# Performance work log

Hardware: AMD Instinct MI355X
Metric: run time of the kernel (lower is better)

## Reference

```python
import jax, jax.numpy as jnp
from jax import lax
import numpy as np

THRESHOLD = 1.25
CURRENT_DECAY = 0.25
VOLTAGE_DECAY = 0.03
TAU_GRAD = 0.03
SCALE_GRAD = 3.0


@jax.custom_vjp
def spike_fn(v):
    # Heaviside spike on membrane voltage (threshold already subtracted)
    return (v >= 0.0).astype(v.dtype)

def _spike_fwd(v):
    return spike_fn(v), v

def _spike_bwd(v, g):
    # slayer-style exponential surrogate gradient around threshold
    surrogate = SCALE_GRAD * jnp.exp(-jnp.abs(v) / TAU_GRAD)
    return (g * surrogate,)

spike_fn.defvjp(_spike_fwd, _spike_bwd)


def cuba_dense(x, v_w, g_w, delay):
    """x: [B, C_in, T] spikes -> [B, C_out, T] spikes.
    Weight-normalized dense synapse + CUBA leaky-integrate-and-fire scan + axonal delay."""
    # weight norm: W = g * v / ||v||_row
    norm = jnp.sqrt(jnp.sum(v_w * v_w, axis=1, keepdims=True))
    W = g_w[:, None] * v_w / norm                       # [O, C]
    z = jnp.einsum('bct,oc->bot', x, W)                 # synaptic current input [B, O, T]
    B, O, T = z.shape
    zT = jnp.transpose(z, (2, 0, 1))                    # [T, B, O]

    def step(carry, zt):
        cur, vol = carry
        cur = cur * (1.0 - CURRENT_DECAY) + zt
        vol = vol * (1.0 - VOLTAGE_DECAY) + cur
        s = spike_fn(vol - THRESHOLD)
        vol = vol * (1.0 - s)                           # reset to zero on spike
        return (cur, vol), s

    init = (jnp.zeros((B, O), z.dtype), jnp.zeros((B, O), z.dtype))
    _, sT = lax.scan(step, init, zT)                    # [T, B, O]
    s = jnp.transpose(sT, (1, 2, 0))                    # [B, O, T]

    # per-neuron integer axonal delay: out[b,n,t] = s[b,n,t-d_n]
    t_idx = jnp.arange(T)[None, :] - delay[:, None]     # [O, T]
    valid = (t_idx >= 0)
    gathered = s[:, jnp.arange(O)[:, None], jnp.clip(t_idx, 0, T - 1)]
    return jnp.where(valid[None, :, :], gathered, jnp.zeros((), s.dtype))


def setup_inputs() -> dict:
    key = jax.random.key(0)
    ks = jax.random.split(key, 10)
    B, C, T = 32, 34 * 34 * 2, 300
    spike = (jax.random.uniform(ks[0], (B, C, T)) < 0.1).astype(jnp.float32)
    v1 = jax.random.normal(ks[1], (512, C), jnp.float32) * 0.1
    g1 = jax.random.uniform(ks[2], (512,), jnp.float32) + 0.5
    v2 = jax.random.normal(ks[3], (512, 512), jnp.float32) * 0.1
    g2 = jax.random.uniform(ks[4], (512,), jnp.float32) + 0.5
    v3 = jax.random.normal(ks[5], (10, 512), jnp.float32) * 0.1
    g3 = jax.random.uniform(ks[6], (10,), jnp.float32) + 0.5
    d1 = jax.random.randint(ks[7], (512,), 0, 8, jnp.int32)
    d2 = jax.random.randint(ks[8], (512,), 0, 8, jnp.int32)
    d3 = jax.random.randint(ks[9], (10,), 0, 8, jnp.int32)
    return {"spike": spike, "v1": v1, "g1": g1, "v2": v2, "g2": g2,
            "v3": v3, "g3": g3, "d1": d1, "d2": d2, "d3": d3}


def reference(spike, v1, g1, v2, g2, v3, g3, d1, d2, d3):
    s1 = cuba_dense(spike, v1, g1, d1)
    s2 = cuba_dense(s1, v2, g2, d2)
    s3 = cuba_dense(s2, v3, g3, d3)
    counts = jnp.stack([jnp.mean(s1), jnp.mean(s2), jnp.mean(s3)]).reshape(1, -1)
    return s3, counts
```

## Files before the change

kernel.cpp:

```cpp
#include <hip/hip_runtime.h>

#define B_   32
#define T_   300
#define C1_  2312
#define O1_  512
#define O2_  512
#define O3_  10
#define M_   (B_*T_)
#define KSPLIT_ 1152


__global__ void calc_f(const float* __restrict__ v, const float* __restrict__ g,
                       double* __restrict__ f, int O, int C) {
    int o = blockIdx.x;
    const float* row = v + (size_t)o * C;
    double s = 0.0;
    for (int c = threadIdx.x; c < C; c += blockDim.x) {
        double x = (double)row[c];
        s += x * x;
    }
    for (int off = 32; off; off >>= 1) s += __shfl_down(s, off);
    __shared__ double wsum[4];
    int lane = threadIdx.x & 63, wv = threadIdx.x >> 6;
    if (lane == 0) wsum[wv] = s;
    __syncthreads();
    if (threadIdx.x == 0) {
        double tot = 0.0;
        for (int i = 0; i < (int)(blockDim.x >> 6); ++i) tot += wsum[i];
        f[o] = (double)g[o] / sqrt(tot);
    }
}

__global__ void transpose_scale(const float* __restrict__ v, const double* __restrict__ f,
                                double* __restrict__ wt, int O, int C, int ldo) {
    __shared__ double tile[32][33];
    int c0 = blockIdx.x * 32, o0 = blockIdx.y * 32;
    int tx = threadIdx.x, ty = threadIdx.y;
    for (int k = 0; k < 4; ++k) {
        int o = o0 + ty + k * 8, c = c0 + tx;
        double val = 0.0;
        if (o < O && c < C) val = (double)v[(size_t)o * C + c] * f[o];
        tile[ty + k * 8][tx] = val;
    }
    __syncthreads();
    for (int k = 0; k < 4; ++k) {
        int c = c0 + ty + k * 8, o = o0 + tx;
        if (c < C && o < O) wt[(size_t)c * ldo + o] = tile[tx][ty + k * 8];
    }
}

__global__ void build_bits(const float* __restrict__ X, unsigned* __restrict__ bits) {
    size_t idx = (size_t)blockIdx.x * 256 + threadIdx.x;
    if (idx >= (size_t)B_ * C1_ * 10) return;
    int t32 = (int)(idx % 10);
    size_t bc = idx / 10;
    const float* src = X + bc * T_ + t32 * 32;
    int nq = (t32 == 9) ? 3 : 8;
    unsigned m = 0;
    for (int q = 0; q < nq; ++q) {
        float4 v = *(const float4*)(src + q * 4);
        if (v.x != 0.f) m |= 1u << (q * 4 + 0);
        if (v.y != 0.f) m |= 1u << (q * 4 + 1);
        if (v.z != 0.f) m |= 1u << (q * 4 + 2);
        if (v.w != 0.f) m |= 1u << (q * 4 + 3);
    }
    bits[idx] = m;
}

__global__ __launch_bounds__(512, 4) void gemm1(const unsigned* __restrict__ Xbits,
                                                const double* __restrict__ Wt,
                                                double* __restrict__ Z0,
                                                double* __restrict__ Z1) {
    __shared__ double Ws[2][16][256];
    int n = blockIdx.x;
    int combo = n & 3;
    int khalf = combo & 1;
    int o0 = (combo >> 1) * 256;
    int i = n >> 2;
    int tb = i % 10;
    int bpair = i / 10;
    int tid = threadIdx.x;
    int w = tid >> 6;
    int lane = tid & 63;
    int b = bpair * 2 + (w >> 2);
    int w8s = __builtin_amdgcn_readfirstlane((w & 3) << 3);
    int cbeg = khalf ? KSPLIT_ : 0;
    int qend = khalf ? C1_ : KSPLIT_;
    const int NT = khalf ? 73 : 72;
    double* __restrict__ Z = khalf ? Z1 : Z0;
    double acc[8][4];
#pragma unroll
    for (int tj = 0; tj < 8; ++tj)
#pragma unroll
        for (int i2 = 0; i2 < 4; ++i2) acc[tj][i2] = 0.0;
    const unsigned* xbp = Xbits + (size_t)b * C1_ * 10 + tb;

    double2 wreg[4];
    unsigned mval, mvaln = 0u;

    auto load_w = [&](int c0) {
#pragma unroll
        for (int h = 0; h < 4; ++h) {
            int idx = h * 512 + tid;
            int r = idx >> 7, od = (idx & 127) * 2;
            int c = c0 + r;
            double2 val; val.x = 0.0; val.y = 0.0;
            if (c < qend) val = *(const double2*)(Wt + (size_t)c * O1_ + o0 + od);
            wreg[h] = val;
        }
    };
    auto load_m = [&](int c0) -> unsigned {
        int c = c0 + lane;
        return (lane < 16 && c < qend) ? xbp[(size_t)c * 10] : 0u;
    };
    auto store_w = [&](int bi) {
#pragma unroll
        for (int h = 0; h < 4; ++h) {
            int idx = h * 512 + tid;
            int r = idx >> 7, od = (idx & 127) * 2;
            *(double2*)(&Ws[bi][r][od]) = wreg[h];
        }
    };

    load_w(cbeg);
    mval = load_m(cbeg);
    store_w(0);
    __syncthreads();
    int cur = 0;
    for (int tile = 0; tile < NT; ++tile) {
        if (tile + 1 < NT) {
            int cn = cbeg + (tile + 1) * 16;
            load_w(cn);
            mvaln = load_m(cn);
        }
#pragma unroll
        for (int k = 0; k < 16; ++k) {
            unsigned smk = (unsigned)__builtin_amdgcn_readlane((int)mval, k);
            unsigned soct = (smk >> w8s) & 0xffu;
            if (soct) {
                double wf[4];
#pragma unroll
                for (int i2 = 0; i2 < 4; ++i2) wf[i2] = Ws[cur][k][lane + 64 * i2];
#pragma unroll
                for (int tj = 0; tj < 8; ++tj) {
                    if (soct & (1u << tj)) {
#pragma unroll
                        for (int i2 = 0; i2 < 4; ++i2) acc[tj][i2] += wf[i2];
                    }
                }
            }
        }
        if (tile + 1 < NT) {
            store_w(cur ^ 1);
            __syncthreads();
        }
        mval = mvaln;
        cur ^= 1;
    }
#pragma unroll
    for (int tj = 0; tj < 8; ++tj) {
        int t = tb * 32 + w8s + tj;
        if (t < T_) {
            double* dst = Z + ((size_t)b * T_ + t) * O1_ + o0;
#pragma unroll
            for (int i2 = 0; i2 < 4; ++i2)
                dst[lane + 64 * i2] = acc[tj][i2];
        }
    }
}

__global__ __launch_bounds__(512, 4) void gemm2s(const unsigned* __restrict__ Sbits,
                                                 const double* __restrict__ Wt,
                                                 double* __restrict__ Z0,
                                                 double* __restrict__ Z1) {
    __shared__ double Ws[2][16][256];
    int n = blockIdx.x;
    int combo = n & 3;
    int khalf = combo & 1;
    int o0 = (combo >> 1) * 256;
    int i = n >> 2;
    int twin = i % 5;
    int b = i / 5;
    int tid = threadIdx.x;
    int w = tid >> 6;
    int lane = tid & 63;
    int w8s = __builtin_amdgcn_readfirstlane((w & 3) << 3);
    int word = twin * 2 + (w >> 2);
    int cbeg = khalf * 256;
    double* __restrict__ Z = khalf ? Z1 : Z0;
    double acc[8][4];
#pragma unroll
    for (int tj = 0; tj < 8; ++tj)
#pragma unroll
        for (int i2 = 0; i2 < 4; ++i2) acc[tj][i2] = 0.0;
    const unsigned* xbp = Sbits + (size_t)b * O1_ * 10 + word;

    double2 wreg[4];
    unsigned mval, mvaln = 0u;

    auto load_w = [&](int c0) {
#pragma unroll
        for (int h = 0; h < 4; ++h) {
            int idx = h * 512 + tid;
            int r = idx >> 7, od = (idx & 127) * 2;
            int c = c0 + r;
            wreg[h] = *(const double2*)(Wt + (size_t)c * O2_ + o0 + od);
        }
    };
    auto load_m = [&](int c0) -> unsigned {
        int c = c0 + lane;
        return (lane < 16) ? xbp[(size_t)c * 10] : 0u;
    };
    auto store_w = [&](int bi) {
#pragma unroll
        for (int h = 0; h < 4; ++h) {
            int idx = h * 512 + tid;
            int r = idx >> 7, od = (idx & 127) * 2;
            *(double2*)(&Ws[bi][r][od]) = wreg[h];
        }
    };

    load_w(cbeg);
    mval = load_m(cbeg);
    store_w(0);
    __syncthreads();
    int cur = 0;
    for (int tile = 0; tile < 16; ++tile) {
        if (tile + 1 < 16) {
            int cn = cbeg + (tile + 1) * 16;
            load_w(cn);
            mvaln = load_m(cn);
        }
#pragma unroll
        for (int k = 0; k < 16; ++k) {
            unsigned smk = (unsigned)__builtin_amdgcn_readlane((int)mval, k);
            unsigned soct = (smk >> w8s) & 0xffu;
            if (soct) {
                double wf[4];
#pragma unroll
                for (int i2 = 0; i2 < 4; ++i2) wf[i2] = Ws[cur][k][lane + 64 * i2];
#pragma unroll
                for (int tj = 0; tj < 8; ++tj) {
                    if (soct & (1u << tj)) {
#pragma unroll
                        for (int i2 = 0; i2 < 4; ++i2) acc[tj][i2] += wf[i2];
                    }
                }
            }
        }
        if (tile + 1 < 16) {
            store_w(cur ^ 1);
            __syncthreads();
        }
        mval = mvaln;
        cur ^= 1;
    }
#pragma unroll
    for (int tj = 0; tj < 8; ++tj) {
        int t = twin * 64 + w * 8 + tj;
        if (t < T_) {
            double* dst = Z + ((size_t)b * T_ + t) * O2_ + o0;
#pragma unroll
            for (int i2 = 0; i2 < 4; ++i2)
                dst[lane + 64 * i2] = acc[tj][i2];
        }
    }
}

__global__ void gemm3(const float* __restrict__ A,
                      const double* __restrict__ Wt,
                      double* __restrict__ Z) {
    __shared__ double w[512 * 16];
    for (int e = threadIdx.x; e < 4096; e += 256)
        ((double2*)w)[e] = ((const double2*)Wt)[e];
    __syncthreads();
    int m = blockIdx.x * 256 + threadIdx.x;
    if (m >= M_) return;
    double acc[O3_];
#pragma unroll
    for (int o = 0; o < O3_; ++o) acc[o] = 0.0;
    const float4* Ar = (const float4*)(A + (size_t)m * 512);
    for (int cq = 0; cq < 128; ++cq) {
        float4 a = Ar[cq];
        float av[4] = {a.x, a.y, a.z, a.w};
#pragma unroll
        for (int u = 0; u < 4; ++u)
#pragma unroll
            for (int o = 0; o < O3_; ++o) acc[o] += (double)av[u] * w[(cq * 4 + u) * 16 + o];
    }
    double* dst = Z + (size_t)m * 16;
#pragma unroll
    for (int o = 0; o < O3_; ++o) dst[o] = acc[o];
}

__global__ void scan12(const double* __restrict__ Za,
                       const double* __restrict__ Zb,
                       const int* __restrict__ delay,
                       float* __restrict__ Sout,
                       unsigned* __restrict__ bitsOut,
                       float* __restrict__ sumOut) {
    int blk = blockIdx.x;
    int o = (blk & 7) * 64 + threadIdx.x;
    int b = blk >> 3;
    size_t base = (size_t)b * T_ * O1_ + o;
    const double* z  = Za + base;
    const double* z2 = Zb ? Zb + base : nullptr;
    float* s = Sout ? Sout + base : nullptr;
    int d = delay[o];
    if (s) for (int t = 0; t < d; ++t) s[(size_t)t * O1_] = 0.f;
    double cur = 0.0, vol = 0.0;
    float cnt = 0.f;
    unsigned bw = 0u;
    for (int t8 = 0; t8 < 296; t8 += 8) {
        double zbuf[8];
#pragma unroll
        for (int u = 0; u < 8; ++u) zbuf[u] = z[(size_t)(t8 + u) * O1_];
        if (z2) {
#pragma unroll
            for (int u = 0; u < 8; ++u) zbuf[u] += z2[(size_t)(t8 + u) * O1_];
        }
#pragma unroll
        for (int u = 0; u < 8; ++u) {
            int t = t8 + u;
            cur = cur * 0.75 + zbuf[u];
            vol = vol * 0.97 + cur;
            float sp = (vol >= 1.25) ? 1.f : 0.f;
            if (sp > 0.f) vol = 0.0;
            int tw = t + d;
            if (tw < T_) {
                if (s) s[(size_t)tw * O1_] = sp;
                cnt += sp;
                if (bitsOut) {
                    if (sp > 0.f) bw |= 1u << (tw & 31);
                    if ((tw & 31) == 31) { bitsOut[((size_t)b * O1_ + o) * 10 + (tw >> 5)] = bw; bw = 0u; }
                }
            }
        }
    }
    {
        double zbuf[4];
#pragma unroll
        for (int u = 0; u < 4; ++u) zbuf[u] = z[(size_t)(296 + u) * O1_];
        if (z2) {
#pragma unroll
            for (int u = 0; u < 4; ++u) zbuf[u] += z2[(size_t)(296 + u) * O1_];
        }
#pragma unroll
        for (int u = 0; u < 4; ++u) {
            int t = 296 + u;
            cur = cur * 0.75 + zbuf[u];
            vol = vol * 0.97 + cur;
            float sp = (vol >= 1.25) ? 1.f : 0.f;
            if (sp > 0.f) vol = 0.0;
            int tw = t + d;
            if (tw < T_) {
                if (s) s[(size_t)tw * O1_] = sp;
                cnt += sp;
                if (bitsOut) {
                    if (sp > 0.f) bw |= 1u << (tw & 31);
                    if ((tw & 31) == 31) { bitsOut[((size_t)b * O1_ + o) * 10 + (tw >> 5)] = bw; bw = 0u; }
                }
            }
        }
    }
    if (bitsOut) bitsOut[((size_t)b * O1_ + o) * 10 + 9] = bw;
    for (int off = 32; off; off >>= 1) cnt += __shfl_down(cnt, off);
    if (threadIdx.x == 0) atomicAdd(sumOut, cnt);
}

__global__ void scan3(const double* __restrict__ Z3,
                      const int* __restrict__ d3,
                      float* __restrict__ out,
                      float* __restrict__ sumOut) {
    __shared__ double zt[T_ * 16];
    int b = blockIdx.x;
    const double2* src = (const double2*)(Z3 + (size_t)b * T_ * 16);
    for (int e = threadIdx.x; e < T_ * 8; e += 64)
        ((double2*)zt)[e] = src[e];
    __syncthreads();
    int o = threadIdx.x;
    if (o < O3_) {
        int d = d3[o];
        float* dst = out + (size_t)b * O3_ * T_ + (size_t)o * T_;
        for (int t = 0; t < d; ++t) dst[t] = 0.f;
        double cur = 0.0, vol = 0.0;
        float cnt = 0.f;
        for (int t = 0; t < T_; ++t) {
            cur = cur * 0.75 + zt[t * 16 + o];
            vol = vol * 0.97 + cur;
            float sp = (vol >= 1.25) ? 1.f : 0.f;
            if (sp > 0.f) vol = 0.0;
            int tw = t + d;
            if (tw < T_) { dst[tw] = sp; cnt += sp; }
        }
        atomicAdd(sumOut, cnt);
    }
}

__global__ void finalize(const float* __restrict__ sums, float* __restrict__ out) {
    if (threadIdx.x == 0) {
        out[0] = (float)((double)sums[0] / (double)(B_ * O1_ * T_));
        out[1] = (float)((double)sums[1] / (double)(B_ * O2_ * T_));
        out[2] = (float)((double)sums[2] / (double)(B_ * O3_ * T_));
    }
}

extern "C" void kernel_launch(void* const* d_in, const int* in_sizes, int n_in,
                              void* d_out, int out_size, void* d_ws, size_t ws_size,
                              hipStream_t stream) {
    const float* spike = (const float*)d_in[0];
    const float* v1 = (const float*)d_in[1];
    const float* g1 = (const float*)d_in[2];
    const float* v2 = (const float*)d_in[3];
    const float* g2 = (const float*)d_in[4];
    const float* v3 = (const float*)d_in[5];
    const float* g3 = (const float*)d_in[6];
    const int* d1 = (const int*)d_in[7];
    const int* d2 = (const int*)d_in[8];
    const int* d3 = (const int*)d_in[9];
    float* out = (float*)d_out;

    double* dw = (double*)d_ws;
    size_t off = 0;
    double* f1  = dw + off; off += 512;
    double* f2  = dw + off; off += 512;
    double* f3  = dw + off; off += 16;
    double* Wt1 = dw + off; off += (size_t)C1_ * O1_;
    double* Wt2 = dw + off; off += 512 * 512;
    double* Wt3 = dw + off; off += 512 * 16;
    double* zA  = dw + off; off += (size_t)M_ * 512;
    double* zB  = dw + off; off += (size_t)M_ * 512;
    double* z3b = dw + off; off += (size_t)M_ * 16;
    float* fw = (float*)(dw + off);
    float* sB    = fw;
    float* sums  = fw + (size_t)M_ * 512;
    unsigned* Xbits = (unsigned*)(fw + (size_t)M_ * 512 + 4);
    unsigned* bits2 = Xbits + (size_t)B_ * C1_ * 10;
    (void)ws_size; (void)out_size; (void)in_sizes; (void)n_in;

    hipMemsetAsync(sums, 0, 4 * sizeof(float), stream);

    build_bits<<<(B_ * C1_ * 10 + 255) / 256, 256, 0, stream>>>(spike, Xbits);

    calc_f<<<512, 256, 0, stream>>>(v1, g1, f1, O1_, C1_);
    calc_f<<<512, 256, 0, stream>>>(v2, g2, f2, O2_, O1_);
    calc_f<<<O3_, 256, 0, stream>>>(v3, g3, f3, O3_, O2_);

    transpose_scale<<<dim3((C1_ + 31) / 32, 16), dim3(32, 8), 0, stream>>>(v1, f1, Wt1, O1_, C1_, O1_);
    transpose_scale<<<dim3(16, 16), dim3(32, 8), 0, stream>>>(v2, f2, Wt2, O2_, O1_, O2_);
    transpose_scale<<<dim3(16, 1), dim3(32, 8), 0, stream>>>(v3, f3, Wt3, O3_, O2_, 16);

    gemm1<<<640, 512, 0, stream>>>(Xbits, Wt1, zA, zB);
    scan12<<<256, 64, 0, stream>>>(zA, zB, d1, nullptr, bits2, sums + 0);
    gemm2s<<<640, 512, 0, stream>>>(bits2, Wt2, zA, zB);
    scan12<<<256, 64, 0, stream>>>(zA, zB, d2, sB, nullptr, sums + 1);
    gemm3<<<(M_ + 255) / 256, 256, 0, stream>>>(sB, Wt3, z3b);
    scan3<<<B_, 64, 0, stream>>>(z3b, d3, out, sums + 2);
    finalize<<<1, 64, 0, stream>>>(sums, out + (size_t)B_ * O3_ * T_);
}
```

Baseline: 794.1 us.

## Drop LDS weight staging in spike GEMMs, read weights directly per active row

Both bit-sparse GEMM kernels stop double-buffering weight tiles through shared memory. They now load each weight row from global memory (served by cache) only when some time bit is set, and accumulate with 2-wide double vectors. The blocks shrink to 256 threads, the second GEMM no longer splits K (so there is one output buffer and scan12 gets a nullptr), and outputs use nontemporal stores. This removes barriers and unconditional tile loads, but depends on L2/L1 hit rates for scattered weight reads and assumes scan12 handles a null second buffer.

```diff
diff --git a/kernel.cpp b/kernel.cpp
--- a/kernel.cpp
+++ b/kernel.cpp
@@ -8,6 +8,8 @@
 #define O3_  10
 #define M_   (B_*T_)
 #define KSPLIT_ 1152
+
+typedef double v2d __attribute__((ext_vector_type(2)));
 
 
 __global__ void calc_f(const float* __restrict__ v, const float* __restrict__ g,
@@ -67,202 +69,128 @@
     bits[idx] = m;
 }
 
-__global__ __launch_bounds__(512, 4) void gemm1(const unsigned* __restrict__ Xbits,
+__global__ __launch_bounds__(256, 5) void gemm1(const unsigned* __restrict__ Xbits,
                                                 const double* __restrict__ Wt,
                                                 double* __restrict__ Z0,
                                                 double* __restrict__ Z1) {
-    __shared__ double Ws[2][16][256];
     int n = blockIdx.x;
     int combo = n & 3;
     int khalf = combo & 1;
     int o0 = (combo >> 1) * 256;
     int i = n >> 2;
     int tb = i % 10;
-    int bpair = i / 10;
+    int b = i / 10;
     int tid = threadIdx.x;
     int w = tid >> 6;
     int lane = tid & 63;
-    int b = bpair * 2 + (w >> 2);
-    int w8s = __builtin_amdgcn_readfirstlane((w & 3) << 3);
+    int w8s = __builtin_amdgcn_readfirstlane(w << 3);
     int cbeg = khalf ? KSPLIT_ : 0;
-    int qend = khalf ? C1_ : KSPLIT_;
-    const int NT = khalf ? 73 : 72;
+    int cend = khalf ? C1_ : KSPLIT_;
+    const int NG = khalf ? 73 : 72;
     double* __restrict__ Z = khalf ? Z1 : Z0;
-    double acc[8][4];
+    v2d acc[8][2];
 #pragma unroll
     for (int tj = 0; tj < 8; ++tj)
 #pragma unroll
-        for (int i2 = 0; i2 < 4; ++i2) acc[tj][i2] = 0.0;
+        for (int i2 = 0; i2 < 2; ++i2) { acc[tj][i2][0] = 0.0; acc[tj][i2][1] = 0.0; }
     const unsigned* xbp = Xbits + (size_t)b * C1_ * 10 + tb;
 
-    double2 wreg[4];
-    unsigned mval, mvaln = 0u;
-
-    auto load_w = [&](int c0) {
-#pragma unroll
-        for (int h = 0; h < 4; ++h) {
-            int idx = h * 512 + tid;
-            int r = idx >> 7, od = (idx & 127) * 2;
-            int c = c0 + r;
-            double2 val; val.x = 0.0; val.y = 0.0;
-            if (c < qend) val = *(const double2*)(Wt + (size_t)c * O1_ + o0 + od);
-            wreg[h] = val;
-        }
-    };
     auto load_m = [&](int c0) -> unsigned {
         int c = c0 + lane;
-        return (lane < 16 && c < qend) ? xbp[(size_t)c * 10] : 0u;
+        return (lane < 16 && c < cend) ? xbp[(size_t)c * 10] : 0u;
     };
-    auto store_w = [&](int bi) {
-#pragma unroll
-        for (int h = 0; h < 4; ++h) {
-            int idx = h * 512 + tid;
-            int r = idx >> 7, od = (idx & 127) * 2;
-            *(double2*)(&Ws[bi][r][od]) = wreg[h];
-        }
-    };
-
-    load_w(cbeg);
-    mval = load_m(cbeg);
-    store_w(0);
-    __syncthreads();
-    int cur = 0;
-    for (int tile = 0; tile < NT; ++tile) {
-        if (tile + 1 < NT) {
-            int cn = cbeg + (tile + 1) * 16;
-            load_w(cn);
-            mvaln = load_m(cn);
-        }
+
+    unsigned mval = load_m(cbeg);
+    int c0 = cbeg;
+    for (int g = 0; g < NG; ++g) {
+        unsigned mnext = (g + 1 < NG) ? load_m(c0 + 16) : 0u;
 #pragma unroll
         for (int k = 0; k < 16; ++k) {
             unsigned smk = (unsigned)__builtin_amdgcn_readlane((int)mval, k);
             unsigned soct = (smk >> w8s) & 0xffu;
             if (soct) {
-                double wf[4];
-#pragma unroll
-                for (int i2 = 0; i2 < 4; ++i2) wf[i2] = Ws[cur][k][lane + 64 * i2];
+                const v2d* wp = (const v2d*)(Wt + (size_t)(c0 + k) * O1_ + o0);
+                v2d wf0 = wp[lane];
+                v2d wf1 = wp[lane + 64];
 #pragma unroll
                 for (int tj = 0; tj < 8; ++tj) {
                     if (soct & (1u << tj)) {
-#pragma unroll
-                        for (int i2 = 0; i2 < 4; ++i2) acc[tj][i2] += wf[i2];
+                        acc[tj][0] += wf0;
+                        acc[tj][1] += wf1;
                     }
                 }
             }
         }
-        if (tile + 1 < NT) {
-            store_w(cur ^ 1);
-            __syncthreads();
-        }
-        mval = mvaln;
-        cur ^= 1;
+        mval = mnext;
+        c0 += 16;
     }
 #pragma unroll
     for (int tj = 0; tj < 8; ++tj) {
         int t = tb * 32 + w8s + tj;
         if (t < T_) {
-            double* dst = Z + ((size_t)b * T_ + t) * O1_ + o0;
-#pragma unroll
-            for (int i2 = 0; i2 < 4; ++i2)
-                dst[lane + 64 * i2] = acc[tj][i2];
-        }
-    }
-}
-
-__global__ __launch_bounds__(512, 4) void gemm2s(const unsigned* __restrict__ Sbits,
+            v2d* dst = (v2d*)(Z + ((size_t)b * T_ + t) * O1_ + o0);
+            __builtin_nontemporal_store(acc[tj][0], dst + lane);
+            __builtin_nontemporal_store(acc[tj][1], dst + lane + 64);
+        }
+    }
+}
+
+__global__ __launch_bounds__(256, 5) void gemm2s(const unsigned* __restrict__ Sbits,
                                                  const double* __restrict__ Wt,
-                                                 double* __restrict__ Z0,
-                                                 double* __restrict__ Z1) {
-    __shared__ double Ws[2][16][256];
+                                                 double* __restrict__ Z) {
     int n = blockIdx.x;
-    int combo = n & 3;
-    int khalf = combo & 1;
-    int o0 = (combo >> 1) * 256;
-    int i = n >> 2;
-    int twin = i % 5;
-    int b = i / 5;
+    int ohalf = n & 1;
+    int o0 = ohalf * 256;
+    int i = n >> 1;
+    int g4 = i % 10;
+    int b = i / 10;
     int tid = threadIdx.x;
     int w = tid >> 6;
     int lane = tid & 63;
-    int w8s = __builtin_amdgcn_readfirstlane((w & 3) << 3);
-    int word = twin * 2 + (w >> 2);
-    int cbeg = khalf * 256;
-    double* __restrict__ Z = khalf ? Z1 : Z0;
-    double acc[8][4];
+    int w8s = __builtin_amdgcn_readfirstlane(w << 3);
+    v2d acc[8][2];
 #pragma unroll
     for (int tj = 0; tj < 8; ++tj)
 #pragma unroll
-        for (int i2 = 0; i2 < 4; ++i2) acc[tj][i2] = 0.0;
-    const unsigned* xbp = Sbits + (size_t)b * O1_ * 10 + word;
-
-    double2 wreg[4];
-    unsigned mval, mvaln = 0u;
-
-    auto load_w = [&](int c0) {
-#pragma unroll
-        for (int h = 0; h < 4; ++h) {
-            int idx = h * 512 + tid;
-            int r = idx >> 7, od = (idx & 127) * 2;
-            int c = c0 + r;
-            wreg[h] = *(const double2*)(Wt + (size_t)c * O2_ + o0 + od);
-        }
-    };
+        for (int i2 = 0; i2 < 2; ++i2) { acc[tj][i2][0] = 0.0; acc[tj][i2][1] = 0.0; }
+    const unsigned* xbp = Sbits + (size_t)b * O1_ * 10 + g4;
+
     auto load_m = [&](int c0) -> unsigned {
         int c = c0 + lane;
         return (lane < 16) ? xbp[(size_t)c * 10] : 0u;
     };
-    auto store_w = [&](int bi) {
-#pragma unroll
-        for (int h = 0; h < 4; ++h) {
-            int idx = h * 512 + tid;
-            int r = idx >> 7, od = (idx & 127) * 2;
-            *(double2*)(&Ws[bi][r][od]) = wreg[h];
-        }
-    };
-
-    load_w(cbeg);
-    mval = load_m(cbeg);
-    store_w(0);
-    __syncthreads();
-    int cur = 0;
-    for (int tile = 0; tile < 16; ++tile) {
-        if (tile + 1 < 16) {
-            int cn = cbeg + (tile + 1) * 16;
-            load_w(cn);
-            mvaln = load_m(cn);
-        }
+
+    unsigned mval = load_m(0);
+    int c0 = 0;
+    for (int g = 0; g < 32; ++g) {
+        unsigned mnext = (g + 1 < 32) ? load_m(c0 + 16) : 0u;
 #pragma unroll
         for (int k = 0; k < 16; ++k) {
             unsigned smk = (unsigned)__builtin_amdgcn_readlane((int)mval, k);
             unsigned soct = (smk >> w8s) & 0xffu;
             if (soct) {
-                double wf[4];
-#pragma unroll
-                for (int i2 = 0; i2 < 4; ++i2) wf[i2] = Ws[cur][k][lane + 64 * i2];
+                const v2d* wp = (const v2d*)(Wt + (size_t)(c0 + k) * O2_ + o0);
+                v2d wf0 = wp[lane];
+                v2d wf1 = wp[lane + 64];
 #pragma unroll
                 for (int tj = 0; tj < 8; ++tj) {
                     if (soct & (1u << tj)) {
-#pragma unroll
-                        for (int i2 = 0; i2 < 4; ++i2) acc[tj][i2] += wf[i2];
+                        acc[tj][0] += wf0;
+                        acc[tj][1] += wf1;
                     }
                 }
             }
         }
-        if (tile + 1 < 16) {
-            store_w(cur ^ 1);
-            __syncthreads();
-        }
-        mval = mvaln;
-        cur ^= 1;
+        mval = mnext;
+        c0 += 16;
     }
 #pragma unroll
     for (int tj = 0; tj < 8; ++tj) {
-        int t = twin * 64 + w * 8 + tj;
+        int t = g4 * 32 + w8s + tj;
         if (t < T_) {
-            double* dst = Z + ((size_t)b * T_ + t) * O2_ + o0;
-#pragma unroll
-            for (int i2 = 0; i2 < 4; ++i2)
-                dst[lane + 64 * i2] = acc[tj][i2];
+            v2d* dst = (v2d*)(Z + ((size_t)b * T_ + t) * O2_ + o0);
+            __builtin_nontemporal_store(acc[tj][0], dst + lane);
+            __builtin_nontemporal_store(acc[tj][1], dst + lane + 64);
         }
     }
 }
@@ -450,10 +378,10 @@
     transpose_scale<<<dim3(16, 16), dim3(32, 8), 0, stream>>>(v2, f2, Wt2, O2_, O1_, O2_);
     transpose_scale<<<dim3(16, 1), dim3(32, 8), 0, stream>>>(v3, f3, Wt3, O3_, O2_, 16);
 
-    gemm1<<<640, 512, 0, stream>>>(Xbits, Wt1, zA, zB);
+    gemm1<<<1280, 256, 0, stream>>>(Xbits, Wt1, zA, zB);
     scan12<<<256, 64, 0, stream>>>(zA, zB, d1, nullptr, bits2, sums + 0);
-    gemm2s<<<640, 512, 0, stream>>>(bits2, Wt2, zA, zB);
-    scan12<<<256, 64, 0, stream>>>(zA, zB, d2, sB, nullptr, sums + 1);
+    gemm2s<<<640, 256, 0, stream>>>(bits2, Wt2, zA);
+    scan12<<<256, 64, 0, stream>>>(zA, nullptr, d2, sB, nullptr, sums + 1);
     gemm3<<<(M_ + 255) / 256, 256, 0, stream>>>(sB, Wt3, z3b);
     scan3<<<B_, 64, 0, stream>>>(z3b, d3, out, sums + 2);
     finalize<<<1, 64, 0, stream>>>(sums, out + (size_t)B_ * O3_ * T_);
```

After: 3.032 ms. +281.8%, slower.

## Restructure gemm1 to stream weights straight into registers with 16-step tiles

Applied to the files above, without the earlier changes.

Rewrites the first spike-gated GEMM so each wave owns 16 timesteps by 128 outputs, using double2 vectors. Weights are loaded directly from global memory into a double-buffered register batch, with no LDS staging and no block-wide barriers. The grid becomes 1280 blocks of 256 threads, and outputs are written with nontemporal stores. The aim is to remove shared-memory traffic and synchronisation. In exchange, each wave fetches its own weight rows from L2, so weight reuse across waves drops. The final prefetch may also read past the end of the weight array.

```diff
diff --git a/kernel.cpp b/kernel.cpp
--- a/kernel.cpp
+++ b/kernel.cpp
@@ -8,6 +8,8 @@
 #define O3_  10
 #define M_   (B_*T_)
 #define KSPLIT_ 1152
+
+typedef double v2d __attribute__((ext_vector_type(2)));
 
 
 __global__ void calc_f(const float* __restrict__ v, const float* __restrict__ g,
@@ -67,104 +69,89 @@
     bits[idx] = m;
 }
 
-__global__ __launch_bounds__(512, 4) void gemm1(const unsigned* __restrict__ Xbits,
+__global__ __launch_bounds__(256, 4) void gemm1(const unsigned* __restrict__ Xbits,
                                                 const double* __restrict__ Wt,
                                                 double* __restrict__ Z0,
                                                 double* __restrict__ Z1) {
-    __shared__ double Ws[2][16][256];
     int n = blockIdx.x;
     int combo = n & 3;
     int khalf = combo & 1;
-    int o0 = (combo >> 1) * 256;
+    int ohalf = combo >> 1;
     int i = n >> 2;
-    int tb = i % 10;
-    int bpair = i / 10;
+    int twp = i % 10;
+    int b = i / 10;
     int tid = threadIdx.x;
     int w = tid >> 6;
     int lane = tid & 63;
-    int b = bpair * 2 + (w >> 2);
-    int w8s = __builtin_amdgcn_readfirstlane((w & 3) << 3);
+    int oq = ohalf * 2 + (w & 1);
+    int tw = twp * 2 + (w >> 1);
+    if (tw >= 19) return;
+    int shift = __builtin_amdgcn_readfirstlane((tw & 1) * 16);
+    int word = tw >> 1;
     int cbeg = khalf ? KSPLIT_ : 0;
-    int qend = khalf ? C1_ : KSPLIT_;
-    const int NT = khalf ? 73 : 72;
+    int cend = khalf ? C1_ : KSPLIT_;
+    const int nb = khalf ? 290 : 288;
     double* __restrict__ Z = khalf ? Z1 : Z0;
-    double acc[8][4];
-#pragma unroll
-    for (int tj = 0; tj < 8; ++tj)
-#pragma unroll
-        for (int i2 = 0; i2 < 4; ++i2) acc[tj][i2] = 0.0;
-    const unsigned* xbp = Xbits + (size_t)b * C1_ * 10 + tb;
-
-    double2 wreg[4];
-    unsigned mval, mvaln = 0u;
-
-    auto load_w = [&](int c0) {
-#pragma unroll
-        for (int h = 0; h < 4; ++h) {
-            int idx = h * 512 + tid;
-            int r = idx >> 7, od = (idx & 127) * 2;
-            int c = c0 + r;
-            double2 val; val.x = 0.0; val.y = 0.0;
-            if (c < qend) val = *(const double2*)(Wt + (size_t)c * O1_ + o0 + od);
-            wreg[h] = val;
-        }
-    };
+    int o0 = oq * 128;
+
+    v2d acc[16];
+#pragma unroll
+    for (int tj = 0; tj < 16; ++tj) { acc[tj][0] = 0.0; acc[tj][1] = 0.0; }
+
+    const unsigned* xbp = Xbits + (size_t)b * C1_ * 10 + word;
     auto load_m = [&](int c0) -> unsigned {
         int c = c0 + lane;
-        return (lane < 16 && c < qend) ? xbp[(size_t)c * 10] : 0u;
-    };
-    auto store_w = [&](int bi) {
-#pragma unroll
-        for (int h = 0; h < 4; ++h) {
-            int idx = h * 512 + tid;
-            int r = idx >> 7, od = (idx & 127) * 2;
-            *(double2*)(&Ws[bi][r][od]) = wreg[h];
-        }
-    };
-
-    load_w(cbeg);
-    mval = load_m(cbeg);
-    store_w(0);
-    __syncthreads();
-    int cur = 0;
-    for (int tile = 0; tile < NT; ++tile) {
-        if (tile + 1 < NT) {
-            int cn = cbeg + (tile + 1) * 16;
-            load_w(cn);
-            mvaln = load_m(cn);
-        }
-#pragma unroll
-        for (int k = 0; k < 16; ++k) {
-            unsigned smk = (unsigned)__builtin_amdgcn_readlane((int)mval, k);
-            unsigned soct = (smk >> w8s) & 0xffu;
-            if (soct) {
-                double wf[4];
-#pragma unroll
-                for (int i2 = 0; i2 < 4; ++i2) wf[i2] = Ws[cur][k][lane + 64 * i2];
-#pragma unroll
-                for (int tj = 0; tj < 8; ++tj) {
-                    if (soct & (1u << tj)) {
-#pragma unroll
-                        for (int i2 = 0; i2 < 4; ++i2) acc[tj][i2] += wf[i2];
+        return (lane < 16 && c < cend) ? xbp[(size_t)c * 10] : 0u;
+    };
+    const v2d* __restrict__ Wv = (const v2d*)(Wt + o0);
+
+    auto load_batch = [&](int cb, v2d wf[4]) {
+#pragma unroll
+        for (int j = 0; j < 4; ++j)
+            wf[j] = Wv[(size_t)(cb + j) * 256 + lane];
+    };
+    auto compute4 = [&](const v2d wf[4], unsigned mv, int kk) {
+#pragma unroll
+        for (int j = 0; j < 4; ++j) {
+            unsigned smk = (unsigned)__builtin_amdgcn_readlane((int)mv, kk + j);
+            unsigned s16 = (smk >> shift) & 0xffffu;
+            if (s16) {
+#pragma unroll
+                for (int nib = 0; nib < 4; ++nib) {
+                    if (s16 & (0xfu << (nib * 4))) {
+#pragma unroll
+                        for (int e = 0; e < 4; ++e) {
+                            int tj = nib * 4 + e;
+                            if (s16 & (1u << tj)) acc[tj] += wf[j];
+                        }
                     }
                 }
             }
         }
-        if (tile + 1 < NT) {
-            store_w(cur ^ 1);
-            __syncthreads();
-        }
-        mval = mvaln;
-        cur ^= 1;
-    }
-#pragma unroll
-    for (int tj = 0; tj < 8; ++tj) {
-        int t = tb * 32 + w8s + tj;
+    };
+
+    unsigned mval = load_m(cbeg);
+    unsigned mnext = load_m(cbeg + 16);
+    v2d wfa[4], wfb[4];
+    load_batch(cbeg, wfa);
+    for (int bt = 0; bt < nb; bt += 2) {
+        int c0 = cbeg + bt * 4;
+        load_batch(c0 + 4, wfb);
+        int kk = (bt & 3) * 4;
+        compute4(wfa, mval, kk);
+        load_batch(c0 + 8, wfa);
+        compute4(wfb, mval, kk + 4);
+        if (kk == 8) {
+            mval = mnext;
+            mnext = load_m(c0 + 24);
+        }
+    }
+#pragma unroll
+    for (int tj = 0; tj < 16; ++tj) {
+        int t = tw * 16 + tj;
         if (t < T_) {
-            double* dst = Z + ((size_t)b * T_ + t) * O1_ + o0;
-#pragma unroll
-            for (int i2 = 0; i2 < 4; ++i2)
-                dst[lane + 64 * i2] = acc[tj][i2];
+            v2d* dst = (v2d*)(Z + ((size_t)b * T_ + t) * O1_ + o0);
+            __builtin_nontemporal_store(acc[tj], dst + lane);
         }
     }
 }
@@ -450,7 +437,7 @@
     transpose_scale<<<dim3(16, 16), dim3(32, 8), 0, stream>>>(v2, f2, Wt2, O2_, O1_, O2_);
     transpose_scale<<<dim3(16, 1), dim3(32, 8), 0, stream>>>(v3, f3, Wt3, O3_, O2_, 16);
 
-    gemm1<<<640, 512, 0, stream>>>(Xbits, Wt1, zA, zB);
+    gemm1<<<1280, 256, 0, stream>>>(Xbits, Wt1, zA, zB);
     scan12<<<256, 64, 0, stream>>>(zA, zB, d1, nullptr, bits2, sums + 0);
     gemm2s<<<640, 512, 0, stream>>>(bits2, Wt2, zA, zB);
     scan12<<<256, 64, 0, stream>>>(zA, zB, d2, sB, nullptr, sums + 1);
```

Result: slower. 1.096 ms (+38.1%).

## Remap spike GEMM warps to 32 timesteps by 64 outputs per lane

Applied to the files above, without the earlier changes.

In both sparse-spike GEMM kernels, each wavefront now owns one 64-output quarter and a full 32-bit word of timesteps, instead of all 256 outputs across 8 timesteps. Every lane loads one weight per input channel and conditionally adds it into up to 32 accumulators, skipping empty bytes of the spike mask. gemm1 now indexes the bit-packed input by batch and 64-step window like gemm2s. The intent is to cut LDS reads per add and to skip zero spike masks at coarser granularity. In exchange there are more per-bit branches, and divergence on the mask is wavefront-uniform but sequential.

```diff
diff --git a/kernel.cpp b/kernel.cpp
--- a/kernel.cpp
+++ b/kernel.cpp
@@ -77,23 +77,22 @@
     int khalf = combo & 1;
     int o0 = (combo >> 1) * 256;
     int i = n >> 2;
-    int tb = i % 10;
-    int bpair = i / 10;
+    int twin = i % 5;
+    int b = i / 5;
     int tid = threadIdx.x;
     int w = tid >> 6;
     int lane = tid & 63;
-    int b = bpair * 2 + (w >> 2);
-    int w8s = __builtin_amdgcn_readfirstlane((w & 3) << 3);
+    int th = w >> 2;
+    int oq = w & 3;
+    int word = twin * 2 + th;
     int cbeg = khalf ? KSPLIT_ : 0;
     int qend = khalf ? C1_ : KSPLIT_;
     const int NT = khalf ? 73 : 72;
     double* __restrict__ Z = khalf ? Z1 : Z0;
-    double acc[8][4];
-#pragma unroll
-    for (int tj = 0; tj < 8; ++tj)
-#pragma unroll
-        for (int i2 = 0; i2 < 4; ++i2) acc[tj][i2] = 0.0;
-    const unsigned* xbp = Xbits + (size_t)b * C1_ * 10 + tb;
+    double acc[32];
+#pragma unroll
+    for (int tj = 0; tj < 32; ++tj) acc[tj] = 0.0;
+    const unsigned* xbp = Xbits + (size_t)b * C1_ * 10 + word;
 
     double2 wreg[4];
     unsigned mval, mvaln = 0u;
@@ -135,17 +134,17 @@
         }
 #pragma unroll
         for (int k = 0; k < 16; ++k) {
-            unsigned smk = (unsigned)__builtin_amdgcn_readlane((int)mval, k);
-            unsigned soct = (smk >> w8s) & 0xffu;
-            if (soct) {
-                double wf[4];
-#pragma unroll
-                for (int i2 = 0; i2 < 4; ++i2) wf[i2] = Ws[cur][k][lane + 64 * i2];
-#pragma unroll
-                for (int tj = 0; tj < 8; ++tj) {
-                    if (soct & (1u << tj)) {
-#pragma unroll
-                        for (int i2 = 0; i2 < 4; ++i2) acc[tj][i2] += wf[i2];
+            unsigned m32 = (unsigned)__builtin_amdgcn_readlane((int)mval, k);
+            if (m32) {
+                double wf = Ws[cur][k][oq * 64 + lane];
+#pragma unroll
+                for (int nb = 0; nb < 4; ++nb) {
+                    if (m32 & (0xffu << (nb * 8))) {
+#pragma unroll
+                        for (int e = 0; e < 8; ++e) {
+                            int tj = nb * 8 + e;
+                            if (m32 & (1u << tj)) acc[tj] += wf;
+                        }
                     }
                 }
             }
@@ -158,13 +157,10 @@
         cur ^= 1;
     }
 #pragma unroll
-    for (int tj = 0; tj < 8; ++tj) {
-        int t = tb * 32 + w8s + tj;
+    for (int tj = 0; tj < 32; ++tj) {
+        int t = twin * 64 + th * 32 + tj;
         if (t < T_) {
-            double* dst = Z + ((size_t)b * T_ + t) * O1_ + o0;
-#pragma unroll
-            for (int i2 = 0; i2 < 4; ++i2)
-                dst[lane + 64 * i2] = acc[tj][i2];
+            Z[((size_t)b * T_ + t) * O1_ + o0 + oq * 64 + lane] = acc[tj];
         }
     }
 }
@@ -184,15 +180,14 @@
     int tid = threadIdx.x;
     int w = tid >> 6;
     int lane = tid & 63;
-    int w8s = __builtin_amdgcn_readfirstlane((w & 3) << 3);
-    int word = twin * 2 + (w >> 2);
+    int th = w >> 2;
+    int oq = w & 3;
+    int word = twin * 2 + th;
     int cbeg = khalf * 256;
     double* __restrict__ Z = khalf ? Z1 : Z0;
-    double acc[8][4];
-#pragma unroll
-    for (int tj = 0; tj < 8; ++tj)
-#pragma unroll
-        for (int i2 = 0; i2 < 4; ++i2) acc[tj][i2] = 0.0;
+    double acc[32];
+#pragma unroll
+    for (int tj = 0; tj < 32; ++tj) acc[tj] = 0.0;
     const unsigned* xbp = Sbits + (size_t)b * O1_ * 10 + word;
 
     double2 wreg[4];
@@ -233,17 +228,17 @@
         }
 #pragma unroll
         for (int k = 0; k < 16; ++k) {
-            unsigned smk = (unsigned)__builtin_amdgcn_readlane((int)mval, k);
-            unsigned soct = (smk >> w8s) & 0xffu;
-            if (soct) {
-                double wf[4];
-#pragma unroll
-                for (int i2 = 0; i2 < 4; ++i2) wf[i2] = Ws[cur][k][lane + 64 * i2];
-#pragma unroll
-                for (int tj = 0; tj < 8; ++tj) {
-                    if (soct & (1u << tj)) {
-#pragma unroll
-                        for (int i2 = 0; i2 < 4; ++i2) acc[tj][i2] += wf[i2];
+            unsigned m32 = (unsigned)__builtin_amdgcn_readlane((int)mval, k);
+            if (m32) {
+                double wf = Ws[cur][k][oq * 64 + lane];
+#pragma unroll
+                for (int nb = 0; nb < 4; ++nb) {
+                    if (m32 & (0xffu << (nb * 8))) {
+#pragma unroll
+                        for (int e = 0; e < 8; ++e) {
+                            int tj = nb * 8 + e;
+                            if (m32 & (1u << tj)) acc[tj] += wf;
+                        }
                     }
                 }
             }
@@ -256,13 +251,10 @@
         cur ^= 1;
     }
 #pragma unroll
-    for (int tj = 0; tj < 8; ++tj) {
-        int t = twin * 64 + w * 8 + tj;
+    for (int tj = 0; tj < 32; ++tj) {
+        int t = twin * 64 + th * 32 + tj;
         if (t < T_) {
-            double* dst = Z + ((size_t)b * T_ + t) * O2_ + o0;
-#pragma unroll
-            for (int i2 = 0; i2 < 4; ++i2)
-                dst[lane + 64 * i2] = acc[tj][i2];
+            Z[((size_t)b * T_ + t) * O2_ + o0 + oq * 64 + lane] = acc[tj];
         }
     }
 }
```

New measurement: 1.905 ms. +139.9%, slower.
